# Optimization experiments

Hardware: AMD Instinct MI355X
Metric: run time of the kernel (lower is better)

Reference implementation:

```python
import jax, jax.numpy as jnp
import numpy as np

M1 = M2 = M3 = 12   # Fourier modes kept per dim
WID = 32            # channel width
NL = 4              # number of Fourier layers
HID = 128           # skip-block hidden
INF = 9             # coord_dim + param_dim


def _gelu(x):
    return jax.nn.gelu(x, approximate=False)  # torch F.gelu default is exact erf


def _spectral_conv3d(x, w1, w2, w3, w4):
    # x: [B, Cin, S, V, T]; weights: [Cin, Cout, M1, M2, M3, 2]
    B, Ci, S, Vd, T = x.shape
    x_ft = jnp.fft.rfftn(x, axes=(-3, -2, -1))  # [B,Ci,S,V,T//2+1] complex64

    def cmul(sub, w):
        wc = w[..., 0] + 1j * w[..., 1]
        return jnp.einsum('bixyz,ioxyz->boxyz', sub, wc)

    Co = w1.shape[1]
    out_ft = jnp.zeros((B, Co, S, Vd, T // 2 + 1), dtype=x_ft.dtype)
    out_ft = out_ft.at[:, :, :M1, :M2, :M3].set(cmul(x_ft[:, :, :M1, :M2, :M3], w1))
    out_ft = out_ft.at[:, :, -M1:, :M2, :M3].set(cmul(x_ft[:, :, -M1:, :M2, :M3], w2))
    out_ft = out_ft.at[:, :, :M1, -M2:, :M3].set(cmul(x_ft[:, :, :M1, -M2:, :M3], w3))
    out_ft = out_ft.at[:, :, -M1:, -M2:, :M3].set(cmul(x_ft[:, :, -M1:, -M2:, :M3], w4))
    return jnp.fft.irfftn(out_ft, s=(S, Vd, T), axes=(-3, -2, -1))


def setup_inputs() -> dict:
    key = jax.random.key(0)
    ks = jax.random.split(key, 24)
    B, S, Vd, T = 4, 64, 64, 64
    scale = 1.0 / (WID * WID)
    spec_shape = (NL, WID, WID, M1, M2, M3, 2)
    inp = {
        'coords': jax.random.uniform(ks[0], (B, S, Vd, T, 3), dtype=jnp.float32),
        'params': jax.random.normal(ks[1], (B, 6), dtype=jnp.float32),
        'lift_w': 0.3 * jax.random.normal(ks[2], (INF, WID), dtype=jnp.float32),
        'lift_b': jnp.zeros((WID,), jnp.float32),
        'spec_w1': scale * jax.random.uniform(ks[3], spec_shape, dtype=jnp.float32),
        'spec_w2': scale * jax.random.uniform(ks[4], spec_shape, dtype=jnp.float32),
        'spec_w3': scale * jax.random.uniform(ks[5], spec_shape, dtype=jnp.float32),
        'spec_w4': scale * jax.random.uniform(ks[6], spec_shape, dtype=jnp.float32),
        'conv_w': 0.15 * jax.random.normal(ks[7], (NL, WID, WID), dtype=jnp.float32),
        'conv_b': jnp.zeros((NL, WID), jnp.float32),
        's1w': 0.3 * jax.random.normal(ks[8], (NL, INF, HID), dtype=jnp.float32),
        's1b': jnp.zeros((NL, HID), jnp.float32),
        's2w': 0.09 * jax.random.normal(ks[9], (NL, HID, HID), dtype=jnp.float32),
        's2b': jnp.zeros((NL, HID), jnp.float32),
        's3w': 0.09 * jax.random.normal(ks[10], (NL, HID, WID), dtype=jnp.float32),
        's3b': jnp.zeros((NL, WID), jnp.float32),
        'p1w': 0.15 * jax.random.normal(ks[11], (WID, WID // 2), dtype=jnp.float32),
        'p1b': jnp.zeros((WID // 2,), jnp.float32),
        'p2w': 0.25 * jax.random.normal(ks[12], (WID // 2, 1), dtype=jnp.float32),
        'p2b': jnp.zeros((1,), jnp.float32),
    }
    return inp


def reference(coords, params, lift_w, lift_b, spec_w1, spec_w2, spec_w3, spec_w4,
              conv_w, conv_b, s1w, s1b, s2w, s2b, s3w, s3b, p1w, p1b, p2w, p2b):
    B, S, Vd, T, _ = coords.shape
    # coordinate lift: broadcast params over grid, concat -> [B,S,V,T,9]
    pexp = jnp.broadcast_to(params[:, None, None, None, :], (B, S, Vd, T, params.shape[-1]))
    z = jnp.concatenate([coords, pexp], axis=-1)
    x = z @ lift_w + lift_b                      # [B,S,V,T,W]
    x = jnp.transpose(x, (0, 4, 1, 2, 3))        # [B,W,S,V,T]
    for i in range(NL):
        x1 = _spectral_conv3d(x, spec_w1[i], spec_w2[i], spec_w3[i], spec_w4[i])
        x2 = jnp.einsum('bixyz,oi->boxyz', x, conv_w[i]) + conv_b[i][None, :, None, None, None]
        xf = _gelu(x1 + x2)
        skip = _gelu(z @ s1w[i] + s1b[i])
        skip = _gelu(skip @ s2w[i] + s2b[i])
        skip = skip @ s3w[i] + s3b[i]            # [B,S,V,T,W]
        x = xf + jnp.transpose(skip, (0, 4, 1, 2, 3))
    x = jnp.transpose(x, (0, 2, 3, 4, 1))        # [B,S,V,T,W]
    h = _gelu(x @ p1w + p1b)
    out = (h @ p2w + p2b)[..., 0]                # [B,S,V,T]
    return out
```

## Files before the change

kernel.cpp:

```cpp
#include <hip/hip_runtime.h>
#include <hip/hip_bf16.h>
#include <math.h>

#define NB   4
#define NC   32
#define SVT  262144
#define VT   4096
#define NLAY 4
#define TWOPI_64 0.09817477042468103f

typedef __attribute__((ext_vector_type(8))) short bf16x8;
typedef __attribute__((ext_vector_type(4))) float f32x4;
typedef __attribute__((ext_vector_type(4))) unsigned short us4;

__device__ __forceinline__ float gelu_f(float x){
    float x2 = x * x;
    float u  = x * __builtin_fmaf(-0.10294322f, x2, -2.30220795f);
    float e  = __builtin_amdgcn_exp2f(u);
    return x * __builtin_amdgcn_rcpf(1.0f + e);
}

__device__ __forceinline__ unsigned short f2bf(float f){
    union { __hip_bfloat16 h; unsigned short u; } cv;
    cv.h = __float2bfloat16(f);
    return cv.u;
}
__device__ __forceinline__ float bf2f(unsigned short u){
    return __uint_as_float(((unsigned int)u) << 16);
}

__global__ __launch_bounds__(256) void k_prep(
    const float* __restrict__ params,
    const float* __restrict__ s1w, const float* __restrict__ s1b,
    const float* __restrict__ s2w, const float* __restrict__ s3w,
    const float* __restrict__ conv_w,
    unsigned short* __restrict__ w2bf,
    unsigned short* __restrict__ w3bf,
    unsigned short* __restrict__ tdft,
    unsigned short* __restrict__ T1h, unsigned short* __restrict__ T1l,
    unsigned short* __restrict__ T2h, unsigned short* __restrict__ T2l,
    float* __restrict__ pbq,
    unsigned short* __restrict__ w1dup,
    unsigned short* __restrict__ wcvh, unsigned short* __restrict__ wcvl)
{
    int g = blockIdx.x * 256 + threadIdx.x;
    if (g < 65536){
        int l = g >> 14, r = g & 16383;
        int c = r >> 7, k = r & 127;
        w2bf[g] = f2bf(s2w[l*16384 + k*128 + c]);
        return;
    }
    g -= 65536;
    if (g < 16384){
        int l = g >> 12, r = g & 4095;
        int c2 = r >> 7, k = r & 127;
        w3bf[g] = f2bf(s3w[l*4096 + k*32 + c2]);
        return;
    }
    g -= 16384;
    if (g < 2048){
        int o = g >> 6, t = g & 63;
        float val = 0.f;
        if (o < 24){
            int kz = o >> 1;
            float ang = (float)((kz * t) & 63) * TWOPI_64;
            float sn, cs; sincosf(ang, &sn, &cs);
            val = (o & 1) ? -sn : cs;
        }
        unsigned short h = f2bf(val);
        tdft[g]        = h;
        tdft[2048 + g] = f2bf(val - bf2f(h));
        return;
    }
    g -= 2048;
    if (g < 8192){
        int col = g >> 6, k1 = g & 63;
        int v = col >> 1, pout = col & 1;
        float val = 0.f;
        if (k1 < 48){
            int ky = k1 >> 1, pin = k1 & 1;
            int kya = (ky < 12) ? ky : ky + 40;
            float ang = (float)((kya * v) & 63) * TWOPI_64;
            float sn, cs; sincosf(ang, &sn, &cs);
            val = pout == 0 ? (pin == 0 ? cs : -sn) : (pin == 0 ? sn : cs);
        }
        unsigned short h = f2bf(val);
        T1h[g] = h;
        T1l[g] = f2bf(val - bf2f(h));
        return;
    }
    g -= 8192;
    if (g < 2048){
        int t = g >> 5, k2 = g & 31;
        float val = 0.f;
        if (k2 < 24){
            int kz = k2 >> 1, part = k2 & 1;
            float wk = (kz == 0) ? 1.f : 2.f;
            float ang = (float)((kz * t) & 63) * TWOPI_64;
            float sn, cs; sincosf(ang, &sn, &cs);
            val = (part ? -sn : cs) * wk * (1.f / 262144.f);
        }
        unsigned short h = f2bf(val);
        T2h[g] = h;
        T2l[g] = f2bf(val - bf2f(h));
        return;
    }
    g -= 2048;
    if (g < 2048){
        int l = g >> 9, b = (g >> 7) & 3, h = g & 127;
        float acc = s1b[l*128 + h];
        #pragma unroll
        for (int j = 0; j < 6; ++j)
            acc += params[b*6 + j] * bf2f(f2bf(s1w[l*1152 + (3 + j)*128 + h]));
        pbq[g] = acc;
        return;
    }
    g -= 2048;
    if (g < 4096){
        int l = g >> 10, rem = g & 1023;
        int h = rem >> 3, slot = rem & 7;
        float val = 0.f;
        if (slot != 3 && slot != 7){
            int row = (slot < 3) ? slot : slot - 4;
            val = bf2f(f2bf(s1w[l*1152 + row*128 + h]));
        }
        w1dup[g] = f2bf(val);
        return;
    }
    g -= 4096;
    if (g < 4096){
        float val = conv_w[g];
        unsigned short h = f2bf(val);
        wcvh[g] = h;
        wcvl[g] = f2bf(val - bf2f(h));
    }
}

__global__ __launch_bounds__(256) void k_lift(
    const float* __restrict__ coords, const float* __restrict__ params,
    const float* __restrict__ lw, const float* __restrict__ lb,
    float* __restrict__ x)
{
    size_t g = (size_t)blockIdx.x * 256 + threadIdx.x;
    int b = (int)(g >> 18);
    size_t p = g & (size_t)(SVT - 1);
    float z[9];
    z[0] = coords[g*3+0]; z[1] = coords[g*3+1]; z[2] = coords[g*3+2];
    #pragma unroll
    for (int j = 0; j < 6; ++j) z[3+j] = params[b*6+j];
    #pragma unroll
    for (int c = 0; c < 32; ++c){
        float acc = lb[c];
        #pragma unroll
        for (int j = 0; j < 9; ++j) acc += z[j] * lw[j*32 + c];
        x[(size_t)(b*32 + c) * SVT + p] = acc;
    }
}

__global__ __launch_bounds__(256) void k_fwdTV(
    const float* __restrict__ x, const unsigned short* __restrict__ tdft,
    float2* __restrict__ X2)
{
    __shared__ __align__(16) unsigned short Ahi[64][72], Alo[64][72];
    __shared__ __align__(16) unsigned short Bhi[32][72], Blo[32][72];
    __shared__ float2 a2[12][66];
    __shared__ float2 wtab[64];
    int tid = threadIdx.x;
    int bc = blockIdx.x >> 6;
    int s  = blockIdx.x & 63;
    if (tid < 64){
        float sn, cs;
        sincosf((float)tid * TWOPI_64, &sn, &cs);
        wtab[tid] = make_float2(cs, sn);
    }
    for (int i = tid; i < 2048; i += 256){
        int o = i >> 6, t = i & 63;
        Bhi[o][t] = tdft[i];
        Blo[o][t] = tdft[2048 + i];
    }
    {
        int row = tid >> 2, c0 = (tid & 3) << 4;
        const float* src = x + (size_t)bc * SVT + (size_t)s * VT + row*64 + c0;
        #pragma unroll
        for (int q = 0; q < 4; ++q){
            float4 v4 = *(const float4*)&src[q*4];
            float vv[4] = {v4.x, v4.y, v4.z, v4.w};
            #pragma unroll
            for (int e = 0; e < 4; ++e){
                unsigned short h = f2bf(vv[e]);
                Ahi[row][c0 + q*4 + e] = h;
                Alo[row][c0 + q*4 + e] = f2bf(vv[e] - bf2f(h));
            }
        }
    }
    __syncthreads();
    int l = tid & 63, w = tid >> 6;
    int lr = l & 15, kg = l >> 4;
    int r0 = w << 4;
    f32x4 acc[2];
    acc[0] = (f32x4){0.f,0.f,0.f,0.f}; acc[1] = (f32x4){0.f,0.f,0.f,0.f};
    #pragma unroll
    for (int kc = 0; kc < 2; ++kc){
        int ko = kc*32 + kg*8;
        bf16x8 ah = *(const bf16x8*)&Ahi[r0 + lr][ko];
        bf16x8 al = *(const bf16x8*)&Alo[r0 + lr][ko];
        #pragma unroll
        for (int n = 0; n < 2; ++n){
            bf16x8 bh = *(const bf16x8*)&Bhi[n*16 + lr][ko];
            bf16x8 bl = *(const bf16x8*)&Blo[n*16 + lr][ko];
            acc[n] = __builtin_amdgcn_mfma_f32_16x16x32_bf16(ah, bh, acc[n], 0, 0, 0);
            acc[n] = __builtin_amdgcn_mfma_f32_16x16x32_bf16(ah, bl, acc[n], 0, 0, 0);
            acc[n] = __builtin_amdgcn_mfma_f32_16x16x32_bf16(al, bh, acc[n], 0, 0, 0);
        }
    }
    #pragma unroll
    for (int n = 0; n < 2; ++n){
        int o = n*16 + lr;
        if (o < 24){
            int kz = o >> 1;
            #pragma unroll
            for (int r = 0; r < 4; ++r){
                int v = r0 + kg*4 + r;
                if (o & 1) a2[kz][v].y = acc[n][r];
                else       a2[kz][v].x = acc[n][r];
            }
        }
    }
    __syncthreads();
    for (int task = tid; task < 288; task += 256){
        int kz = task % 12;
        int ky = task / 12;
        int kya = (ky < 12) ? ky : ky + 40;
        float re = 0.f, im = 0.f;
        for (int v = 0; v < 64; ++v){
            float2 wv = wtab[(kya * v) & 63];
            float2 a  = a2[kz][v];
            re += a.x * wv.x + a.y * wv.y;
            im += a.y * wv.x - a.x * wv.y;
        }
        X2[((size_t)(bc*12 + kz) * 24 + ky) * 64 + s] = make_float2(re, im);
    }
}

__global__ __launch_bounds__(256) void k_fwdS(
    const float2* __restrict__ X2, float2* __restrict__ X3)
{
    __shared__ float2 cin[32][65];
    __shared__ float2 wtab[64];
    int tid = threadIdx.x;
    if (tid < 64){
        float sn, cs; sincosf((float)tid * TWOPI_64, &sn, &cs);
        wtab[tid] = make_float2(cs, sn);
    }
    int rbase = blockIdx.x * 32;
    for (int i = tid; i < 2048; i += 256){
        int row = i >> 6, s = i & 63;
        cin[row][s] = X2[(size_t)(rbase + row) * 64 + s];
    }
    __syncthreads();
    int row = tid & 31;
    int r = rbase + row;
    int kxg = tid >> 5;
    int kxs[3];
    #pragma unroll
    for (int j = 0; j < 3; ++j){ int kxi = kxg*3 + j; kxs[j] = (kxi < 12) ? kxi : kxi + 40; }
    float re[3] = {0,0,0}, im[3] = {0,0,0};
    for (int s = 0; s < 64; ++s){
        float2 cv = cin[row][s];
        #pragma unroll
        for (int j = 0; j < 3; ++j){
            float2 wv = wtab[(kxs[j] * s) & 63];
            re[j] += cv.x * wv.x + cv.y * wv.y;
            im[j] += cv.y * wv.x - cv.x * wv.y;
        }
    }
    int bc = r / 288; int kz = (r / 24) % 12; int ky = r % 24;
    #pragma unroll
    for (int j = 0; j < 3; ++j){
        int kxi = kxg*3 + j;
        X3[(size_t)bc * 6912 + (size_t)kxi * 288 + ky * 12 + kz] = make_float2(re[j], im[j]);
    }
}

__global__ __launch_bounds__(256) void k_modemix(
    const float2* __restrict__ X3,
    const float* __restrict__ w1, const float* __restrict__ w2,
    const float* __restrict__ w3, const float* __restrict__ w4,
    int layer, float2* __restrict__ Y)
{
    __shared__ float2 wlds[32][64];
    int tid = threadIdx.x;
    int m   = tid & 63;
    int b   = tid >> 6;
    int corner = blockIdx.y >> 3;
    int o0     = (blockIdx.y & 7) * 4;
    int moff0  = blockIdx.x * 64;
    const float* wsrc = (corner==0 ? w1 : corner==1 ? w2 : corner==2 ? w3 : w4)
                        + (size_t)layer * 3538944;
    int moff = moff0 + m;
    int m1  = moff / 144;
    int rem = moff - m1 * 144;
    int kx  = m1 + ((corner == 1 || corner == 3) ? 12 : 0);
    int mode_g = kx * 288 + rem + ((corner >= 2) ? 144 : 0);

    float xr[32], xi[32];
    const float2* xp = X3 + (size_t)b * 32 * 6912 + mode_g;
    #pragma unroll
    for (int i = 0; i < 32; ++i){
        float2 a = xp[(size_t)i * 6912];
        xr[i] = a.x; xi[i] = a.y;
    }
    for (int oo = 0; oo < 4; ++oo){
        int o = o0 + oo;
        __syncthreads();
        for (int j = tid; j < 2048; j += 256){
            int i = j >> 6, mm = j & 63;
            wlds[i][mm] = *(const float2*)&wsrc[((size_t)(i*32 + o) * 1728 + moff0 + mm) * 2];
        }
        __syncthreads();
        float re = 0.f, im = 0.f;
        #pragma unroll
        for (int i = 0; i < 32; ++i){
            float2 wv = wlds[i][m];
            re += xr[i]*wv.x - xi[i]*wv.y;
            im += xr[i]*wv.y + xi[i]*wv.x;
        }
        Y[(size_t)(b*32 + o) * 6912 + mode_g] = make_float2(re, im);
    }
}

__global__ __launch_bounds__(256) void k_invS(
    const float2* __restrict__ Y, float2* __restrict__ Z1)
{
    __shared__ float2 yin[24][24];
    __shared__ float2 wtab[64];
    int tid = threadIdx.x;
    if (tid < 64){
        float sn, cs; sincosf((float)tid * TWOPI_64, &sn, &cs);
        wtab[tid] = make_float2(cs, sn);
    }
    int bo = blockIdx.x / 12;
    int kz = blockIdx.x % 12;
    for (int i = tid; i < 576; i += 256){
        int kx = i / 24, ky = i % 24;
        yin[kx][ky] = Y[(size_t)bo * 6912 + (size_t)kx * 288 + ky * 12 + kz];
    }
    __syncthreads();
    int s = tid & 63;
    int kyg = tid >> 6;
    float re[6] = {0,0,0,0,0,0}, im[6] = {0,0,0,0,0,0};
    for (int kxi = 0; kxi < 24; ++kxi){
        int kxa = (kxi < 12) ? kxi : kxi + 40;
        float2 wv = wtab[(kxa * s) & 63];
        #pragma unroll
        for (int j = 0; j < 6; ++j){
            float2 a = yin[kxi][kyg*6 + j];
            re[j] += a.x * wv.x - a.y * wv.y;
            im[j] += a.x * wv.y + a.y * wv.x;
        }
    }
    #pragma unroll
    for (int j = 0; j < 6; ++j){
        int ky = kyg*6 + j;
        Z1[((size_t)(bo*12 + kz) * 64 + s) * 24 + ky] = make_float2(re[j], im[j]);
    }
}

__global__ __launch_bounds__(256) void k_cinvVT(
    const float* __restrict__ xin, const float2* __restrict__ Z1,
    const unsigned short* __restrict__ T2h, const unsigned short* __restrict__ T2l,
    const unsigned short* __restrict__ wcvh, const unsigned short* __restrict__ wcvl,
    const float* __restrict__ cb, int layer, float* __restrict__ xout)
{
    __shared__ __align__(16) unsigned short XT[2][256][40];
    __shared__ __align__(16) unsigned short A2h[128][40], A2l[128][40];
    __shared__ float2 wtab[64];
    int tid = threadIdx.x;
    int vg = blockIdx.x & 15;
    int s  = (blockIdx.x >> 4) & 63;
    int b  = blockIdx.x >> 10;
    if (tid < 64){
        float sn, cs; sincosf((float)tid * TWOPI_64, &sn, &cs);
        wtab[tid] = make_float2(cs, sn);
    }
    {
        int row = tid >> 1, half = tid & 1;
        us4 z = (us4){0,0,0,0};
        *(us4*)&A2h[row][24 + half*4] = z;
        *(us4*)&A2l[row][24 + half*4] = z;
    }
    {
        const float* xp = xin + (size_t)b*32*SVT + (size_t)s*VT + (size_t)vg*256 + tid;
        #pragma unroll
        for (int q = 0; q < 4; ++q){
            bf16x8 ph, pl;
            #pragma unroll
            for (int e = 0; e < 8; ++e){
                float v = xp[(size_t)(q*8 + e) * SVT];
                unsigned short h = f2bf(v);
                ph[e] = (short)h;
                pl[e] = (short)f2bf(v - bf2f(h));
            }
            *(bf16x8*)&XT[0][tid][q*8] = ph;
            *(bf16x8*)&XT[1][tid][q*8] = pl;
        }
    }
    __syncthreads();
    #pragma unroll
    for (int j = 0; j < 6; ++j){
        int task = tid + j*256;
        int o = task / 48, rem = task % 48;
        int kz = rem >> 2, vloc = rem & 3;
        int v = vg*4 + vloc;
        const float2* zp = Z1 + ((size_t)((b*32 + o)*12 + kz) * 64 + s) * 24;
        float re = 0.f, im = 0.f;
        #pragma unroll
        for (int ky = 0; ky < 24; ++ky){
            int kya = (ky < 12) ? ky : ky + 40;
            float2 wv = wtab[(kya * v) & 63];
            float2 a = zp[ky];
            re += a.x * wv.x - a.y * wv.y;
            im += a.x * wv.y + a.y * wv.x;
        }
        int row = o*4 + vloc;
        unsigned short hr = f2bf(re), hm = f2bf(im);
        A2h[row][2*kz  ] = hr; A2l[row][2*kz  ] = f2bf(re - bf2f(hr));
        A2h[row][2*kz+1] = hm; A2l[row][2*kz+1] = f2bf(im - bf2f(hm));
    }
    __syncthreads();
    int l = tid & 63, w = tid >> 6, lr = l & 15, kg = l >> 4;
    f32x4 dcv[2][4];
    #pragma unroll
    for (int ot = 0; ot < 2; ++ot){
        bf16x8 ah = *(const bf16x8*)&wcvh[layer*1024 + (ot*16 + lr)*32 + kg*8];
        bf16x8 al = *(const bf16x8*)&wcvl[layer*1024 + (ot*16 + lr)*32 + kg*8];
        #pragma unroll
        for (int ptt = 0; ptt < 4; ++ptt){
            bf16x8 bh = *(const bf16x8*)&XT[0][w*64 + ptt*16 + lr][kg*8];
            bf16x8 bl = *(const bf16x8*)&XT[1][w*64 + ptt*16 + lr][kg*8];
            f32x4 d = (f32x4){0.f,0.f,0.f,0.f};
            d = __builtin_amdgcn_mfma_f32_16x16x32_bf16(ah, bh, d, 0, 0, 0);
            d = __builtin_amdgcn_mfma_f32_16x16x32_bf16(ah, bl, d, 0, 0, 0);
            d = __builtin_amdgcn_mfma_f32_16x16x32_bf16(al, bh, d, 0, 0, 0);
            dcv[ot][ptt] = d;
        }
    }
    __syncthreads();
    float* x2s = (float*)&XT[0][0][0];
    #pragma unroll
    for (int ot = 0; ot < 2; ++ot)
        #pragma unroll
        for (int ptt = 0; ptt < 4; ++ptt)
            #pragma unroll
            for (int r = 0; r < 4; ++r)
                x2s[(ot*16 + kg*4 + r)*266 + w*64 + ptt*16 + lr] = dcv[ot][ptt][r];
    f32x4 dt[2][4];
    #pragma unroll
    for (int rt = 0; rt < 2; ++rt){
        bf16x8 ah = *(const bf16x8*)&A2h[w*32 + rt*16 + lr][kg*8];
        bf16x8 al = *(const bf16x8*)&A2l[w*32 + rt*16 + lr][kg*8];
        #pragma unroll
        for (int n = 0; n < 4; ++n){
            bf16x8 bh = *(const bf16x8*)&T2h[(n*16 + lr)*32 + kg*8];
            bf16x8 bl = *(const bf16x8*)&T2l[(n*16 + lr)*32 + kg*8];
            f32x4 d = (f32x4){0.f,0.f,0.f,0.f};
            d = __builtin_amdgcn_mfma_f32_16x16x32_bf16(ah, bh, d, 0, 0, 0);
            d = __builtin_amdgcn_mfma_f32_16x16x32_bf16(ah, bl, d, 0, 0, 0);
            d = __builtin_amdgcn_mfma_f32_16x16x32_bf16(al, bh, d, 0, 0, 0);
            dt[rt][n] = d;
        }
    }
    __syncthreads();
    size_t outb = (size_t)b*32*SVT + (size_t)s*VT + (size_t)vg*256;
    #pragma unroll
    for (int rt = 0; rt < 2; ++rt){
        int o = 8*w + rt*4 + kg;
        float cbv = cb[layer*32 + o];
        #pragma unroll
        for (int n = 0; n < 4; ++n){
            #pragma unroll
            for (int r = 0; r < 4; ++r){
                int pt = r*64 + n*16 + lr;
                float val = dt[rt][n][r] + x2s[o*266 + pt] + cbv;
                xout[outb + (size_t)o*SVT + pt] = gelu_f(val);
            }
        }
    }
}

template<int LAST>
__global__ __launch_bounds__(512, 8) void k_skip(
    const float* __restrict__ coords,
    const unsigned short* __restrict__ w1dup, const float* __restrict__ pbq,
    const unsigned short* __restrict__ w2bf, const float* __restrict__ s2b,
    const unsigned short* __restrict__ w3bf, const float* __restrict__ s3b,
    int layer, float* __restrict__ xio,
    const float* __restrict__ p1w, const float* __restrict__ p1b,
    const float* __restrict__ p2w, const float* __restrict__ p2b,
    float* __restrict__ out)
{
    __shared__ __align__(16) unsigned short A1[128][136];
    __shared__ __align__(16) unsigned short zst[8][16][8];

    int tid = threadIdx.x;
    size_t g0 = (size_t)blockIdx.x * 128;
    int b = (int)(g0 >> 18);
    const unsigned short* w2g = w2bf + (size_t)layer * 16384;
    const unsigned short* w3g = w3bf + (size_t)layer * 4096;
    const unsigned short* w1g = w1dup + (size_t)layer * 1024;
    const float* pbg = pbq + layer*512 + b*128;
    const float* b2g = s2b + layer*128;

    int l  = tid & 63;
    int w  = tid >> 6;
    int lr = l & 15;
    int kg = l >> 4;

    if (l < 16){
        size_t g = g0 + (size_t)w*16 + l;
        float z0 = coords[g*3+0], z1 = coords[g*3+1], z2 = coords[g*3+2];
        unsigned short h0 = f2bf(z0), h1 = f2bf(z1), h2 = f2bf(z2);
        bf16x8 pk;
        pk[0] = (short)h0; pk[1] = (short)h1; pk[2] = (short)h2; pk[3] = 0;
        pk[4] = (short)f2bf(z0 - bf2f(h0));
        pk[5] = (short)f2bf(z1 - bf2f(h1));
        pk[6] = (short)f2bf(z2 - bf2f(h2));
        pk[7] = 0;
        *(bf16x8*)&zst[w][l][0] = pk;
    }
    bf16x8 bz;
    if (kg == 0) bz = *(const bf16x8*)&zst[w][lr][0];
    else         bz = (bf16x8){0,0,0,0,0,0,0,0};

    {
        f32x4 accB[8];
        #pragma unroll
        for (int m = 0; m < 8; ++m) accB[m] = (f32x4){0.f,0.f,0.f,0.f};
        #pragma unroll
        for (int m = 0; m < 8; ++m){
            bf16x8 af = *(const bf16x8*)&w1g[(m*16 + lr)*8];
            accB[m] = __builtin_amdgcn_mfma_f32_16x16x32_bf16(af, bz, accB[m], 0, 0, 0);
        }
        #pragma unroll
        for (int m = 0; m < 8; ++m){
            int c0 = m*16 + kg*4;
            float4 bb = *(const float4*)&pbg[c0];
            us4 pk4;
            pk4[0] = f2bf(gelu_f(accB[m][0] + bb.x));
            pk4[1] = f2bf(gelu_f(accB[m][1] + bb.y));
            pk4[2] = f2bf(gelu_f(accB[m][2] + bb.z));
            pk4[3] = f2bf(gelu_f(accB[m][3] + bb.w));
            *(us4*)&A1[w*16 + lr][c0] = pk4;
        }
    }
    __syncthreads();

    f32x4 accC[8];
    #pragma unroll
    for (int pt = 0; pt < 8; ++pt) accC[pt] = (f32x4){0.f,0.f,0.f,0.f};
    #pragma unroll
    for (int kc = 0; kc < 4; ++kc){
        int ko = kc*32 + kg*8;
        bf16x8 a0 = *(const bf16x8*)&w2g[(w*16 + lr)*128 + ko];
        #pragma unroll
        for (int pt = 0; pt < 8; ++pt){
            bf16x8 bb = *(const bf16x8*)&A1[pt*16 + lr][ko];
            accC[pt] = __builtin_amdgcn_mfma_f32_16x16x32_bf16(a0, bb, accC[pt], 0, 0, 0);
        }
    }
    __syncthreads();
    {
        int c0 = w*16 + kg*4;
        float4 bb = *(const float4*)&b2g[c0];
        #pragma unroll
        for (int pt = 0; pt < 8; ++pt){
            us4 pk4;
            pk4[0] = f2bf(gelu_f(accC[pt][0] + bb.x));
            pk4[1] = f2bf(gelu_f(accC[pt][1] + bb.y));
            pk4[2] = f2bf(gelu_f(accC[pt][2] + bb.z));
            pk4[3] = f2bf(gelu_f(accC[pt][3] + bb.w));
            *(us4*)&A1[pt*16 + lr][c0] = pk4;
        }
    }
    __syncthreads();

    int nD  = w & 1;
    int pt0 = (w >> 1) * 2;
    float b3v = s3b[layer*32 + nD*16 + lr];
    f32x4 c3[2];
    c3[0] = (f32x4){0.f,0.f,0.f,0.f}; c3[1] = (f32x4){0.f,0.f,0.f,0.f};
    #pragma unroll
    for (int kc = 0; kc < 4; ++kc){
        int ko = kc*32 + kg*8;
        bf16x8 bw3 = *(const bf16x8*)&w3g[(nD*16 + lr)*128 + ko];
        bf16x8 aa0 = *(const bf16x8*)&A1[(pt0    )*16 + lr][ko];
        bf16x8 aa1 = *(const bf16x8*)&A1[(pt0 + 1)*16 + lr][ko];
        c3[0] = __builtin_amdgcn_mfma_f32_16x16x32_bf16(aa0, bw3, c3[0], 0, 0, 0);
        c3[1] = __builtin_amdgcn_mfma_f32_16x16x32_bf16(aa1, bw3, c3[1], 0, 0, 0);
    }
    __syncthreads();

    float* outsT = (float*)&A1[0][0];
    float* hs    = outsT + 4224;
    float* p1wS  = outsT + 6400;
    float* smB   = outsT + 6912;
    {
        int c2 = nD*16 + lr;
        #pragma unroll
        for (int q = 0; q < 2; ++q){
            int p0 = (pt0 + q)*16 + kg*4;
            float4 v4;
            v4.x = c3[q][0] + b3v; v4.y = c3[q][1] + b3v;
            v4.z = c3[q][2] + b3v; v4.w = c3[q][3] + b3v;
            *(float4*)&outsT[c2*132 + p0] = v4;
        }
    }
    if (LAST){
        for (int i = tid; i < 512; i += 512) p1wS[i] = p1w[i];
        if (tid < 512) { if (tid < 512 && tid < 512) {} }
        for (int i = tid; i < 512; i += 512) {}
        if (tid < 16){ smB[tid] = p1b[tid]; smB[16 + tid] = p2w[tid]; }
        if (tid == 32) smB[32] = p2b[0];
        if (tid >= 64 && tid < 64+512-512) {}
        if (tid < 512 && tid < 512) p1wS[tid] = p1w[tid];
    }
    __syncthreads();

    {
        int c  = tid >> 4;
        int pg = tid & 15;
        size_t prel = (g0 & (size_t)(SVT - 1)) + (size_t)pg*8;
        float* gp = xio + (((size_t)(b*32 + c)) << 18) + prel;
        float* op = &outsT[c*132 + pg*8];
        #pragma unroll
        for (int i = 0; i < 8; i += 4){
            float4 xv = *(const float4*)&gp[i];
            float4 ov = *(const float4*)&op[i];
            ov.x += xv.x; ov.y += xv.y; ov.z += xv.z; ov.w += xv.w;
            if (LAST) *(float4*)&op[i] = ov;
            else      *(float4*)&gp[i] = ov;
        }
    }
    if (LAST){
        __syncthreads();
        {
            int p  = tid & 127;
            int jq = tid >> 7;
            float h[4];
            #pragma unroll
            for (int j = 0; j < 4; ++j) h[j] = smB[jq*4 + j];
            for (int c = 0; c < 32; ++c){
                float xv = outsT[c*132 + p];
                #pragma unroll
                for (int j = 0; j < 4; ++j) h[j] += xv * p1wS[c*16 + jq*4 + j];
            }
            #pragma unroll
            for (int j = 0; j < 4; ++j) hs[p*17 + jq*4 + j] = h[j];
        }
        __syncthreads();
        if (tid < 128){
            float acc = smB[32];
            #pragma unroll
            for (int j = 0; j < 16; ++j) acc += gelu_f(hs[tid*17 + j]) * smB[16 + j];
            out[g0 + tid] = acc;
        }
    }
}

extern "C" void kernel_launch(void* const* d_in, const int* in_sizes, int n_in,
                              void* d_out, int out_size, void* d_ws, size_t ws_size,
                              hipStream_t stream)
{
    (void)in_sizes; (void)n_in; (void)out_size; (void)ws_size;
    const float* coords = (const float*)d_in[0];
    const float* params = (const float*)d_in[1];
    const float* lift_w = (const float*)d_in[2];
    const float* lift_b = (const float*)d_in[3];
    const float* sw1    = (const float*)d_in[4];
    const float* sw2    = (const float*)d_in[5];
    const float* sw3    = (const float*)d_in[6];
    const float* sw4    = (const float*)d_in[7];
    const float* conv_w = (const float*)d_in[8];
    const float* conv_b = (const float*)d_in[9];
    const float* s1w    = (const float*)d_in[10];
    const float* s1b    = (const float*)d_in[11];
    const float* s2w    = (const float*)d_in[12];
    const float* s2b    = (const float*)d_in[13];
    const float* s3w    = (const float*)d_in[14];
    const float* s3b    = (const float*)d_in[15];
    const float* p1w    = (const float*)d_in[16];
    const float* p1b    = (const float*)d_in[17];
    const float* p2w    = (const float*)d_in[18];
    const float* p2b    = (const float*)d_in[19];
    float* out = (float*)d_out;

    char* ws = (char*)d_ws;
    float*  xA = (float*)(ws);
    float2* X2 = (float2*)(ws + 134217728ull);
    float2* X3 = (float2*)(ws + 153092096ull);
    float2* Yb = (float2*)(ws + 160169984ull);
    unsigned short* w2bf  = (unsigned short*)(ws + 167247872ull);
    unsigned short* w3bf  = (unsigned short*)(ws + 167378944ull);
    unsigned short* tdft  = (unsigned short*)(ws + 167411712ull);
    unsigned short* T1h   = (unsigned short*)(ws + 167419904ull);
    unsigned short* T1l   = (unsigned short*)(ws + 167436288ull);
    unsigned short* T2h   = (unsigned short*)(ws + 167452672ull);
    unsigned short* T2l   = (unsigned short*)(ws + 167456768ull);
    float*          pbq   = (float*)(ws + 167460864ull);
    unsigned short* w1dup = (unsigned short*)(ws + 167469056ull);
    unsigned short* wcvh  = (unsigned short*)(ws + 167477248ull);
    unsigned short* wcvl  = (unsigned short*)(ws + 167485440ull);

    k_prep<<<408, 256, 0, stream>>>(params, s1w, s1b, s2w, s3w, conv_w,
                                    w2bf, w3bf, tdft, T1h, T1l, T2h, T2l,
                                    pbq, w1dup, wcvh, wcvl);
    k_lift<<<4096, 256, 0, stream>>>(coords, params, lift_w, lift_b, xA);

    for (int l = 0; l < NLAY; ++l){
        k_fwdTV<<<8192, 256, 0, stream>>>(xA, tdft, X2);
        k_fwdS<<<1152, 256, 0, stream>>>(X2, X3);
        dim3 gmm(27, 32);
        k_modemix<<<gmm, 256, 0, stream>>>(X3, sw1, sw2, sw3, sw4, l, Yb);
        k_invS<<<1536, 256, 0, stream>>>(Yb, X2);
        k_cinvVT<<<4096, 256, 0, stream>>>(xA, X2, T2h, T2l, wcvh, wcvl,
                                           conv_b, l, xA);
        if (l < NLAY - 1)
            k_skip<0><<<8192, 512, 0, stream>>>(coords, w1dup, pbq,
                w2bf, s2b, w3bf, s3b, l, xA, p1w, p1b, p2w, p2b, out);
        else
            k_skip<1><<<8192, 512, 0, stream>>>(coords, w1dup, pbq,
                w2bf, s2b, w3bf, s3b, l, xA, p1w, p1b, p2w, p2b, out);
    }
}
```

Measured before the change: 1.553 ms.

## Compute forward V-axis DFT in k_fwdTV with split-bf16 MFMA instead of scalar loop

The scalar per-thread V-direction DFT loop in k_fwdTV (288 tasks over 256 threads, each doing 64 complex MACs from an LDS twiddle table) is replaced by a matrix multiply on MFMA units. The T-DFT result is stored as hi/lo bf16 in a padded 16-row staging tile, and a precomputed real-valued DFT matrix (T3h/T3l, built in k_prep) is applied with three MFMAs per k-chunk to keep near-fp32 accuracy. The aim is to remove the serial tail of the scalar loop, where a second pass of only 32 tasks leaves most threads idle. Separately, k_skip's A1 row stride is shrunk to 132 and read with two 8-byte LDS loads, and some dead code in the LAST branch is cleaned up.

```diff
diff --git a/kernel.cpp b/kernel.cpp
--- a/kernel.cpp
+++ b/kernel.cpp
@@ -27,6 +27,15 @@
 }
 __device__ __forceinline__ float bf2f(unsigned short u){
     return __uint_as_float(((unsigned int)u) << 16);
+}
+
+__device__ __forceinline__ bf16x8 lds8(const unsigned short* p){
+    us4 a = *(const us4*)p;
+    us4 b = *(const us4*)(p + 4);
+    bf16x8 r;
+    r[0]=(short)a[0]; r[1]=(short)a[1]; r[2]=(short)a[2]; r[3]=(short)a[3];
+    r[4]=(short)b[0]; r[5]=(short)b[1]; r[6]=(short)b[2]; r[7]=(short)b[3];
+    return r;
 }
 
 __global__ __launch_bounds__(256) void k_prep(
@@ -41,7 +50,8 @@
     unsigned short* __restrict__ T2h, unsigned short* __restrict__ T2l,
     float* __restrict__ pbq,
     unsigned short* __restrict__ w1dup,
-    unsigned short* __restrict__ wcvh, unsigned short* __restrict__ wcvl)
+    unsigned short* __restrict__ wcvh, unsigned short* __restrict__ wcvl,
+    unsigned short* __restrict__ T3h, unsigned short* __restrict__ T3l)
 {
     int g = blockIdx.x * 256 + threadIdx.x;
     if (g < 65536){
@@ -133,6 +143,21 @@
         unsigned short h = f2bf(val);
         wcvh[g] = h;
         wcvl[g] = f2bf(val - bf2f(h));
+        return;
+    }
+    g -= 4096;
+    if (g < 6144){
+        int row = g >> 7, k = g & 127;
+        int ky = row >> 1, pin = row & 1;
+        int v = k >> 1, part = k & 1;
+        int kya = (ky < 12) ? ky : ky + 40;
+        float ang = (float)((kya * v) & 63) * TWOPI_64;
+        float sn, cs; sincosf(ang, &sn, &cs);
+        float val = (pin == 0) ? (part == 0 ? cs : sn)
+                               : (part == 0 ? -sn : cs);
+        unsigned short h = f2bf(val);
+        T3h[g] = h;
+        T3l[g] = f2bf(val - bf2f(h));
     }
 }
 
@@ -159,24 +184,23 @@
 
 __global__ __launch_bounds__(256) void k_fwdTV(
     const float* __restrict__ x, const unsigned short* __restrict__ tdft,
+    const unsigned short* __restrict__ T3h, const unsigned short* __restrict__ T3l,
     float2* __restrict__ X2)
 {
     __shared__ __align__(16) unsigned short Ahi[64][72], Alo[64][72];
     __shared__ __align__(16) unsigned short Bhi[32][72], Blo[32][72];
-    __shared__ float2 a2[12][66];
-    __shared__ float2 wtab[64];
+    __shared__ __align__(16) unsigned short Ast_h[16][136], Ast_l[16][136];
     int tid = threadIdx.x;
     int bc = blockIdx.x >> 6;
     int s  = blockIdx.x & 63;
-    if (tid < 64){
-        float sn, cs;
-        sincosf((float)tid * TWOPI_64, &sn, &cs);
-        wtab[tid] = make_float2(cs, sn);
-    }
     for (int i = tid; i < 2048; i += 256){
         int o = i >> 6, t = i & 63;
         Bhi[o][t] = tdft[i];
         Blo[o][t] = tdft[2048 + i];
+    }
+    for (int i = tid; i < 544; i += 256){
+        int r = 12 + i / 136, c = i % 136;
+        Ast_h[r][c] = 0; Ast_l[r][c] = 0;
     }
     {
         int row = tid >> 2, c0 = (tid & 3) << 4;
@@ -217,28 +241,40 @@
     for (int n = 0; n < 2; ++n){
         int o = n*16 + lr;
         if (o < 24){
-            int kz = o >> 1;
+            int kz = o >> 1, part = o & 1;
             #pragma unroll
             for (int r = 0; r < 4; ++r){
                 int v = r0 + kg*4 + r;
-                if (o & 1) a2[kz][v].y = acc[n][r];
-                else       a2[kz][v].x = acc[n][r];
+                float val = acc[n][r];
+                unsigned short h = f2bf(val);
+                Ast_h[kz][2*v + part] = h;
+                Ast_l[kz][2*v + part] = f2bf(val - bf2f(h));
             }
         }
     }
     __syncthreads();
-    for (int task = tid; task < 288; task += 256){
-        int kz = task % 12;
-        int ky = task / 12;
-        int kya = (ky < 12) ? ky : ky + 40;
-        float re = 0.f, im = 0.f;
-        for (int v = 0; v < 64; ++v){
-            float2 wv = wtab[(kya * v) & 63];
-            float2 a  = a2[kz][v];
-            re += a.x * wv.x + a.y * wv.y;
-            im += a.y * wv.x - a.x * wv.y;
-        }
-        X2[((size_t)(bc*12 + kz) * 24 + ky) * 64 + s] = make_float2(re, im);
+    if (w < 3){
+        f32x4 d = (f32x4){0.f,0.f,0.f,0.f};
+        #pragma unroll
+        for (int kc = 0; kc < 4; ++kc){
+            int ko = kc*32 + kg*8;
+            bf16x8 ah = lds8(&Ast_h[lr][ko]);
+            bf16x8 al = lds8(&Ast_l[lr][ko]);
+            bf16x8 bh = *(const bf16x8*)&T3h[(w*16 + lr)*128 + ko];
+            bf16x8 bl = *(const bf16x8*)&T3l[(w*16 + lr)*128 + ko];
+            d = __builtin_amdgcn_mfma_f32_16x16x32_bf16(ah, bh, d, 0, 0, 0);
+            d = __builtin_amdgcn_mfma_f32_16x16x32_bf16(ah, bl, d, 0, 0, 0);
+            d = __builtin_amdgcn_mfma_f32_16x16x32_bf16(al, bh, d, 0, 0, 0);
+        }
+        int colg = w*16 + lr;
+        int ky = colg >> 1, pin = colg & 1;
+        float* xf = (float*)X2;
+        #pragma unroll
+        for (int r = 0; r < 4; ++r){
+            int kz = kg*4 + r;
+            if (kz < 12)
+                xf[(((size_t)(bc*12 + kz) * 24 + ky) * 64 + s) * 2 + pin] = d[r];
+        }
     }
 }
 
@@ -499,7 +535,7 @@
     const float* __restrict__ p2w, const float* __restrict__ p2b,
     float* __restrict__ out)
 {
-    __shared__ __align__(16) unsigned short A1[128][136];
+    __shared__ __align__(16) unsigned short A1[128][132];
     __shared__ __align__(16) unsigned short zst[8][16][8];
 
     int tid = threadIdx.x;
@@ -564,7 +600,7 @@
         bf16x8 a0 = *(const bf16x8*)&w2g[(w*16 + lr)*128 + ko];
         #pragma unroll
         for (int pt = 0; pt < 8; ++pt){
-            bf16x8 bb = *(const bf16x8*)&A1[pt*16 + lr][ko];
+            bf16x8 bb = lds8(&A1[pt*16 + lr][ko]);
             accC[pt] = __builtin_amdgcn_mfma_f32_16x16x32_bf16(a0, bb, accC[pt], 0, 0, 0);
         }
     }
@@ -593,8 +629,8 @@
     for (int kc = 0; kc < 4; ++kc){
         int ko = kc*32 + kg*8;
         bf16x8 bw3 = *(const bf16x8*)&w3g[(nD*16 + lr)*128 + ko];
-        bf16x8 aa0 = *(const bf16x8*)&A1[(pt0    )*16 + lr][ko];
-        bf16x8 aa1 = *(const bf16x8*)&A1[(pt0 + 1)*16 + lr][ko];
+        bf16x8 aa0 = lds8(&A1[(pt0    )*16 + lr][ko]);
+        bf16x8 aa1 = lds8(&A1[(pt0 + 1)*16 + lr][ko]);
         c3[0] = __builtin_amdgcn_mfma_f32_16x16x32_bf16(aa0, bw3, c3[0], 0, 0, 0);
         c3[1] = __builtin_amdgcn_mfma_f32_16x16x32_bf16(aa1, bw3, c3[1], 0, 0, 0);
     }
@@ -616,13 +652,9 @@
         }
     }
     if (LAST){
-        for (int i = tid; i < 512; i += 512) p1wS[i] = p1w[i];
-        if (tid < 512) { if (tid < 512 && tid < 512) {} }
-        for (int i = tid; i < 512; i += 512) {}
+        p1wS[tid] = p1w[tid];
         if (tid < 16){ smB[tid] = p1b[tid]; smB[16 + tid] = p2w[tid]; }
         if (tid == 32) smB[32] = p2b[0];
-        if (tid >= 64 && tid < 64+512-512) {}
-        if (tid < 512 && tid < 512) p1wS[tid] = p1w[tid];
     }
     __syncthreads();
 
@@ -710,14 +742,16 @@
     unsigned short* w1dup = (unsigned short*)(ws + 167469056ull);
     unsigned short* wcvh  = (unsigned short*)(ws + 167477248ull);
     unsigned short* wcvl  = (unsigned short*)(ws + 167485440ull);
-
-    k_prep<<<408, 256, 0, stream>>>(params, s1w, s1b, s2w, s3w, conv_w,
+    unsigned short* T3h   = (unsigned short*)(ws + 167493632ull);
+    unsigned short* T3l   = (unsigned short*)(ws + 167505920ull);
+
+    k_prep<<<432, 256, 0, stream>>>(params, s1w, s1b, s2w, s3w, conv_w,
                                     w2bf, w3bf, tdft, T1h, T1l, T2h, T2l,
-                                    pbq, w1dup, wcvh, wcvl);
+                                    pbq, w1dup, wcvh, wcvl, T3h, T3l);
     k_lift<<<4096, 256, 0, stream>>>(coords, params, lift_w, lift_b, xA);
 
     for (int l = 0; l < NLAY; ++l){
-        k_fwdTV<<<8192, 256, 0, stream>>>(xA, tdft, X2);
+        k_fwdTV<<<8192, 256, 0, stream>>>(xA, tdft, T3h, T3l, X2);
         k_fwdS<<<1152, 256, 0, stream>>>(X2, X3);
         dim3 gmm(27, 32);
         k_modemix<<<gmm, 256, 0, stream>>>(X3, sw1, sw2, sw3, sw4, l, Yb);
```

Measured after the change: 1.500 ms. 1.04x faster.
